# Kernel optimization log

Hardware: AMD Instinct MI355X
Metric: run time of the kernel (lower is better)

Reference implementation:

```python
import jax, jax.numpy as jnp
import numpy as np
import math

N = 20000      # nodes
E = 640000     # edges (avg degree 32)
G = 128        # g_dim (input features)
H1 = 128       # rgcn output dim
H2 = 128       # transformer output dim
R = 8          # num_relations


def setup_inputs() -> dict:
    key = jax.random.key(0)
    ks = jax.random.split(key, 12)
    x = jax.random.normal(ks[0], (N, G), dtype=jnp.float32)
    edge_index = jax.random.randint(ks[1], (2, E), 0, N)
    edge_type = jax.random.randint(ks[2], (E,), 0, R)
    s_in = 1.0 / math.sqrt(G)
    s_h1 = 1.0 / math.sqrt(H1)
    return {
        'x': x,
        'edge_index': edge_index,
        'edge_type': edge_type,
        # RGCNConv params (per-relation weights + root weight + bias)
        'rgcn_weight': jax.random.normal(ks[3], (R, G, H1), dtype=jnp.float32) * s_in,
        'rgcn_root': jax.random.normal(ks[4], (G, H1), dtype=jnp.float32) * s_in,
        'rgcn_bias': jnp.zeros((H1,), dtype=jnp.float32),
        # TransformerConv params (heads=1): query/key/value + skip linear
        'Wq': jax.random.normal(ks[5], (H1, H2), dtype=jnp.float32) * s_h1,
        'bq': jnp.zeros((H2,), dtype=jnp.float32),
        'Wk': jax.random.normal(ks[6], (H1, H2), dtype=jnp.float32) * s_h1,
        'bk': jnp.zeros((H2,), dtype=jnp.float32),
        'Wv': jax.random.normal(ks[7], (H1, H2), dtype=jnp.float32) * s_h1,
        'bv': jnp.zeros((H2,), dtype=jnp.float32),
        'Ws': jax.random.normal(ks[8], (H1, H2), dtype=jnp.float32) * s_h1,
        'bs': jnp.zeros((H2,), dtype=jnp.float32),
    }


def reference(x, edge_index, edge_type, rgcn_weight, rgcn_root, rgcn_bias,
              Wq, bq, Wk, bk, Wv, bv, Ws, bs):
    n = x.shape[0]
    src, dst = edge_index[0], edge_index[1]

    # ---- RGCNConv (aggr='mean' per relation, root weight + bias) ----
    # transform nodes by every relation, then gather per-edge message
    xr = jnp.einsum('ni,rio->nro', x, rgcn_weight)          # [N, R, H1]
    msg = xr[src, edge_type]                                # [E, H1]
    # per (dst, relation) edge counts for mean aggregation
    cnt = jnp.zeros((n, rgcn_weight.shape[0]), x.dtype).at[dst, edge_type].add(1.0)
    denom = jnp.maximum(cnt[dst, edge_type], 1.0)[:, None]  # [E, 1]
    agg = jnp.zeros((n, rgcn_weight.shape[2]), x.dtype).at[dst].add(msg / denom)
    h = agg + x @ rgcn_root + rgcn_bias
    h = jax.nn.relu(h)

    # ---- TransformerConv (heads=1, concat, root_weight=True) ----
    d = Wq.shape[1]
    q = h @ Wq + bq                                          # [N, H2]
    k = h @ Wk + bk
    v = h @ Wv + bv
    score = jnp.sum(q[dst] * k[src], axis=-1) / math.sqrt(d) # [E]
    # softmax over incoming edges of each destination node
    smax = jax.ops.segment_max(score, dst, num_segments=n)   # [N]
    e = jnp.exp(score - smax[dst])                           # [E]
    den = jax.ops.segment_sum(e, dst, num_segments=n)        # [N]
    alpha = e / jnp.maximum(den[dst], 1e-16)                 # [E]
    out = jax.ops.segment_sum(alpha[:, None] * v[src], dst, num_segments=n)
    out = out + h @ Ws + bs                                  # skip connection
    return jax.nn.relu(out)
```

## Files before the change

kernel.cpp:

```cpp
#include <hip/hip_runtime.h>

typedef unsigned short u16;
typedef unsigned int u32;
typedef __attribute__((ext_vector_type(8))) short short8;
typedef __attribute__((ext_vector_type(4))) float f32x4;

#define NN 20000
#define EE 640000
#define SCAN_BLOCKS 80

__device__ inline u16 f2bf(float f) {
    u32 x = __float_as_uint(f);
    return (u16)((x + 0x7FFFu + ((x >> 16) & 1u)) >> 16);
}
__device__ inline float lo16(u32 w) { return __uint_as_float(w << 16); }
__device__ inline float hi16(u32 w) { return __uint_as_float(w & 0xFFFF0000u); }
__device__ inline u32 packbf(float a, float b) { return ((u32)f2bf(b) << 16) | (u32)f2bf(a); }

#define ZP_N (NN * 8)
#define CX_N (NN * 32)
#define WP_N (128 * 1152 + 4 * 128 * 128 + 512)
__global__ __launch_bounds__(256) void prep_all(const float* __restrict__ x,
                                                const float* rw, const float* root,
                                                const float* Wq, const float* Wk,
                                                const float* Wv, const float* Ws,
                                                const float* bq, const float* bk,
                                                const float* bv, const float* bs,
                                                int* __restrict__ cnt, u16* __restrict__ xb,
                                                u16* wt1, u16* wt2, float* bcat) {
    int idx = blockIdx.x * 256 + threadIdx.x;
    if (idx < ZP_N) {
        cnt[idx] = 0;
        return;
    }
    idx -= ZP_N;
    if (idx < CX_N) {
        float4 v = *(const float4*)(x + (size_t)idx * 4);
        uint2 o;
        o.x = packbf(v.x, v.y);
        o.y = packbf(v.z, v.w);
        *(uint2*)(xb + (size_t)idx * 4) = o;
        return;
    }
    idx -= CX_N;
    const int S1 = 128 * 1152, S2 = 4 * 128 * 128;
    if (idx < S1) {
        int o = idx / 1152, k = idx - o * 1152;
        float v = (k < 1024) ? rw[k * 128 + o] : root[(k - 1024) * 128 + o];
        wt1[idx] = f2bf(v);
    } else if (idx < S1 + S2) {
        int j = idx - S1;
        int y = j >> 14, rem = j & 16383, o = rem >> 7, i = rem & 127;
        const float* W = (y == 0) ? Wq : (y == 1) ? Wk : (y == 2) ? Wv : Ws;
        wt2[j] = f2bf(W[i * 128 + o]);
    } else if (idx < S1 + S2 + 512) {
        int j = idx - (S1 + S2);
        int y = j >> 7, c = j & 127;
        const float* b = (y == 0) ? bq : (y == 1) ? bk : (y == 2) ? bv : bs;
        bcat[j] = b[c];
    }
}

__global__ void count_rank(const int* __restrict__ ei, const int* __restrict__ et,
                           int* __restrict__ cnt, int* __restrict__ rank) {
    int base = blockIdx.x * 1024 + threadIdx.x;
#pragma unroll
    for (int j = 0; j < 4; j++) {
        int e = base + j * 256;
        if (e < EE) {
            int dst = ei[EE + e];
            int r = et[e];
            rank[e] = atomicAdd(&cnt[dst * 8 + r], 1);
        }
    }
}

__global__ __launch_bounds__(256) void scan_phase1(const int* __restrict__ cnt,
                                                   int* __restrict__ deg_pref,
                                                   int* __restrict__ blk_sums) {
    __shared__ int lds[256];
    int t = threadIdx.x;
    int n = blockIdx.x * 256 + t;
    int d = 0;
    if (n < NN) {
        int4 c0 = *(const int4*)(cnt + n * 8);
        int4 c1 = *(const int4*)(cnt + n * 8 + 4);
        d = c0.x + c0.y + c0.z + c0.w + c1.x + c1.y + c1.z + c1.w;
    }
    lds[t] = d;
    __syncthreads();
    for (int o = 1; o < 256; o <<= 1) {
        int v = (t >= o) ? lds[t - o] : 0;
        __syncthreads();
        lds[t] += v;
        __syncthreads();
    }
    if (n < NN) deg_pref[n] = lds[t];
    if (t == 255) blk_sums[blockIdx.x] = lds[255];
}

__global__ void scan_phase2(int* __restrict__ blk_sums) {
    __shared__ int lds[128];
    int t = threadIdx.x;
    int v = (t < SCAN_BLOCKS) ? blk_sums[t] : 0;
    lds[t] = v;
    __syncthreads();
    for (int o = 1; o < 128; o <<= 1) {
        int a = (t >= o) ? lds[t - o] : 0;
        __syncthreads();
        lds[t] += a;
        __syncthreads();
    }
    if (t < SCAN_BLOCKS) blk_sums[t] = lds[t] - v;
}

__global__ __launch_bounds__(256) void scan_phase3(const int* __restrict__ cnt,
                                                   const int* __restrict__ deg_pref,
                                                   const int* __restrict__ blk_sums,
                                                   int* __restrict__ row_off,
                                                   int* __restrict__ srt) {
    int n = blockIdx.x * 256 + threadIdx.x;
    if (n >= NN) return;
    int4 c0 = *(const int4*)(cnt + n * 8);
    int4 c1 = *(const int4*)(cnt + n * 8 + 4);
    int deg = c0.x + c0.y + c0.z + c0.w + c1.x + c1.y + c1.z + c1.w;
    int start = blk_sums[blockIdx.x] + deg_pref[n] - deg;
    row_off[n] = start;
    int sub = start;
    int o[8];
    o[0] = sub; sub += c0.x;
    o[1] = sub; sub += c0.y;
    o[2] = sub; sub += c0.z;
    o[3] = sub; sub += c0.w;
    o[4] = sub; sub += c1.x;
    o[5] = sub; sub += c1.y;
    o[6] = sub; sub += c1.z;
    o[7] = sub; sub += c1.w;
    *(int4*)(srt + n * 8) = make_int4(o[0], o[1], o[2], o[3]);
    *(int4*)(srt + n * 8 + 4) = make_int4(o[4], o[5], o[6], o[7]);
    if (n == NN - 1) row_off[NN] = sub;
}

__global__ void scatter_kernel(const int* __restrict__ ei, const int* __restrict__ et,
                               const int* __restrict__ srt, const int* __restrict__ rank,
                               int* __restrict__ es) {
    int base = blockIdx.x * 1024 + threadIdx.x;
#pragma unroll
    for (int j = 0; j < 4; j++) {
        int e = base + j * 256;
        if (e < EE) {
            int dst = ei[EE + e];
            int src = ei[e];
            int r = et[e];
            es[srt[dst * 8 + r] + rank[e]] = src;
        }
    }
}

__global__ __launch_bounds__(256) void rgcn_agg(const u16* __restrict__ xb,
                                                const int* __restrict__ srt,
                                                const int* __restrict__ cnt,
                                                const int* __restrict__ es,
                                                u16* __restrict__ pre) {
    int gid = blockIdx.x * 16 + (threadIdx.x >> 4);
    int lane = threadIdx.x & 15;
    if (gid >= NN * 9) return;
    int node = gid / 9;
    int slot = gid - node * 9;
    long prebase = (long)node * 1152;
    if (slot == 8) {
        uint4 xv = *(const uint4*)(xb + (long)node * 128 + lane * 8);
        *(uint4*)(pre + prebase + 1024 + lane * 8) = xv;
        return;
    }
    int c = cnt[node * 8 + slot];
    int p0 = srt[node * 8 + slot];
    float inv = 1.0f / (float)(c > 1 ? c : 1);
    float a0 = 0.f, a1 = 0.f, a2 = 0.f, a3 = 0.f, a4 = 0.f, a5 = 0.f, a6 = 0.f, a7 = 0.f;
    int i = 0;
    for (; i + 4 <= c; i += 4) {
        int s0 = es[p0 + i], s1 = es[p0 + i + 1], s2 = es[p0 + i + 2], s3 = es[p0 + i + 3];
        uint4 w0 = *(const uint4*)(xb + (long)s0 * 128 + lane * 8);
        uint4 w1 = *(const uint4*)(xb + (long)s1 * 128 + lane * 8);
        uint4 w2 = *(const uint4*)(xb + (long)s2 * 128 + lane * 8);
        uint4 w3 = *(const uint4*)(xb + (long)s3 * 128 + lane * 8);
        a0 += (lo16(w0.x) + lo16(w1.x)) + (lo16(w2.x) + lo16(w3.x));
        a1 += (hi16(w0.x) + hi16(w1.x)) + (hi16(w2.x) + hi16(w3.x));
        a2 += (lo16(w0.y) + lo16(w1.y)) + (lo16(w2.y) + lo16(w3.y));
        a3 += (hi16(w0.y) + hi16(w1.y)) + (hi16(w2.y) + hi16(w3.y));
        a4 += (lo16(w0.z) + lo16(w1.z)) + (lo16(w2.z) + lo16(w3.z));
        a5 += (hi16(w0.z) + hi16(w1.z)) + (hi16(w2.z) + hi16(w3.z));
        a6 += (lo16(w0.w) + lo16(w1.w)) + (lo16(w2.w) + lo16(w3.w));
        a7 += (hi16(w0.w) + hi16(w1.w)) + (hi16(w2.w) + hi16(w3.w));
    }
    for (; i < c; i++) {
        int s = es[p0 + i];
        uint4 w = *(const uint4*)(xb + (long)s * 128 + lane * 8);
        a0 += lo16(w.x); a1 += hi16(w.x); a2 += lo16(w.y); a3 += hi16(w.y);
        a4 += lo16(w.z); a5 += hi16(w.z); a6 += lo16(w.w); a7 += hi16(w.w);
    }
    uint4 ow;
    ow.x = packbf(a0 * inv, a1 * inv);
    ow.y = packbf(a2 * inv, a3 * inv);
    ow.z = packbf(a4 * inv, a5 * inv);
    ow.w = packbf(a6 * inv, a7 * inv);
    *(uint4*)(pre + prebase + slot * 128 + lane * 8) = ow;
}

__global__ __launch_bounds__(256) void gemm_bm32(const u16* __restrict__ A,
                                                 const u16* __restrict__ Bt,
                                                 const float* __restrict__ bias,
                                                 u16* __restrict__ C, int rows) {
    __shared__ u16 As[32 * 136];
    __shared__ u16 Bs[128 * 136];
    int tid = threadIdx.x;
    int w = tid >> 6;
    int lane = tid & 63;
    int quad = lane >> 4;
    int ml = lane & 15;
    int mt = w & 1;
    int nq = w >> 1;
    int block_m = blockIdx.x * 32;

    f32x4 acc[4];
#pragma unroll
    for (int i = 0; i < 4; i++) acc[i] = (f32x4){0.f, 0.f, 0.f, 0.f};

    int rbase = tid >> 4;
    int cb = (tid & 15) * 8;

    for (int kb = 0; kb < 1152; kb += 128) {
#pragma unroll
        for (int rep = 0; rep < 2; rep++) {
            int r = rbase + rep * 16;
            int gr = block_m + r;
            short8 val = {};
            if (gr < rows) val = *(const short8*)(A + (long)gr * 1152 + kb + cb);
            *(short8*)(As + r * 136 + cb) = val;
        }
#pragma unroll
        for (int rep = 0; rep < 8; rep++) {
            int r = rbase + rep * 16;
            short8 val = *(const short8*)(Bt + (long)r * 1152 + kb + cb);
            *(short8*)(Bs + r * 136 + cb) = val;
        }
        __syncthreads();
#pragma unroll
        for (int ks = 0; ks < 4; ks++) {
            short8 af = *(const short8*)(As + (mt * 16 + ml) * 136 + ks * 32 + quad * 8);
#pragma unroll
            for (int nt = 0; nt < 4; nt++) {
                short8 bfr = *(const short8*)(Bs + (nq * 64 + nt * 16 + ml) * 136 + ks * 32 + quad * 8);
                acc[nt] = __builtin_amdgcn_mfma_f32_16x16x32_bf16(af, bfr, acc[nt], 0, 0, 0);
            }
        }
        __syncthreads();
    }
#pragma unroll
    for (int nt = 0; nt < 4; nt++) {
        int col = nq * 64 + nt * 16 + ml;
        float bv = bias[col];
#pragma unroll
        for (int i = 0; i < 4; i++) {
            int gr = block_m + mt * 16 + quad * 4 + i;
            if (gr < rows) {
                float vv = fmaxf(acc[nt][i] + bv, 0.f);
                C[(long)gr * 128 + col] = f2bf(vv);
            }
        }
    }
}

__global__ __launch_bounds__(256) void gemm_kernel(const u16* __restrict__ A, int lda,
                                                   const u16* __restrict__ Bt, int ldbt,
                                                   const float* __restrict__ bias,
                                                   u16* __restrict__ C, int ldc,
                                                   int rows, int K, int relu,
                                                   long long yBt, long long yC, long long yBias) {
    Bt += blockIdx.y * yBt;
    C += blockIdx.y * yC;
    bias += blockIdx.y * yBias;
    __shared__ u16 As[64 * 136];
    __shared__ u16 Bs[128 * 136];
    int tid = threadIdx.x;
    int w = tid >> 6;
    int lane = tid & 63;
    int quad = lane >> 4;
    int ml = lane & 15;
    int block_m = blockIdx.x * 64;

    f32x4 acc[8];
#pragma unroll
    for (int i = 0; i < 8; i++) acc[i] = (f32x4){0.f, 0.f, 0.f, 0.f};

    int rbase = tid >> 4;
    int cb = (tid & 15) * 8;

    for (int kb = 0; kb < K; kb += 128) {
#pragma unroll
        for (int rep = 0; rep < 4; rep++) {
            int r = rbase + rep * 16;
            int gr = block_m + r;
            short8 val = {};
            if (gr < rows) val = *(const short8*)(A + (long)gr * lda + kb + cb);
            *(short8*)(As + r * 136 + cb) = val;
        }
#pragma unroll
        for (int rep = 0; rep < 8; rep++) {
            int r = rbase + rep * 16;
            short8 val = *(const short8*)(Bt + (long)r * ldbt + kb + cb);
            *(short8*)(Bs + r * 136 + cb) = val;
        }
        __syncthreads();
#pragma unroll
        for (int ks = 0; ks < 4; ks++) {
            short8 af = *(const short8*)(As + (w * 16 + ml) * 136 + ks * 32 + quad * 8);
#pragma unroll
            for (int nt = 0; nt < 8; nt++) {
                short8 bfr = *(const short8*)(Bs + (nt * 16 + ml) * 136 + ks * 32 + quad * 8);
                acc[nt] = __builtin_amdgcn_mfma_f32_16x16x32_bf16(af, bfr, acc[nt], 0, 0, 0);
            }
        }
        __syncthreads();
    }
#pragma unroll
    for (int nt = 0; nt < 8; nt++) {
        int col = nt * 16 + ml;
        float bv = bias[col];
#pragma unroll
        for (int i = 0; i < 4; i++) {
            int gr = block_m + w * 16 + quad * 4 + i;
            if (gr < rows) {
                float vv = acc[nt][i] + bv;
                if (relu) vv = fmaxf(vv, 0.f);
                C[(long)gr * ldc + col] = f2bf(vv);
            }
        }
    }
}

__global__ __launch_bounds__(256) void attn_kernel(const u16* __restrict__ q, const u16* __restrict__ k,
                                                   const u16* __restrict__ v, const u16* __restrict__ skip,
                                                   const int* __restrict__ row_off, const int* __restrict__ es,
                                                   float* __restrict__ out) {
    int node = blockIdx.x * 16 + (threadIdx.x >> 4);
    int lane = threadIdx.x & 15;
    if (node >= NN) return;
    int p0 = row_off[node], p1 = row_off[node + 1];
    uint4 qw = *(const uint4*)(q + (long)node * 128 + lane * 8);
    float q0 = lo16(qw.x), q1 = hi16(qw.x), q2 = lo16(qw.y), q3 = hi16(qw.y);
    float q4 = lo16(qw.z), q5 = hi16(qw.z), q6 = lo16(qw.w), q7 = hi16(qw.w);
    const float SC = 0.08838834764831845f;
    float m = -INFINITY, l = 0.f;
    float a0 = 0.f, a1 = 0.f, a2 = 0.f, a3 = 0.f, a4 = 0.f, a5 = 0.f, a6 = 0.f, a7 = 0.f;
    int p = p0;
    for (; p + 4 <= p1; p += 4) {
        int s0 = es[p], s1 = es[p + 1], s2 = es[p + 2], s3 = es[p + 3];
        uint4 k0 = *(const uint4*)(k + (long)s0 * 128 + lane * 8);
        uint4 k1 = *(const uint4*)(k + (long)s1 * 128 + lane * 8);
        uint4 k2 = *(const uint4*)(k + (long)s2 * 128 + lane * 8);
        uint4 k3 = *(const uint4*)(k + (long)s3 * 128 + lane * 8);
        uint4 v0 = *(const uint4*)(v + (long)s0 * 128 + lane * 8);
        uint4 v1 = *(const uint4*)(v + (long)s1 * 128 + lane * 8);
        uint4 v2 = *(const uint4*)(v + (long)s2 * 128 + lane * 8);
        uint4 v3 = *(const uint4*)(v + (long)s3 * 128 + lane * 8);
        float t0 = q0 * lo16(k0.x) + q1 * hi16(k0.x) + q2 * lo16(k0.y) + q3 * hi16(k0.y) +
                   q4 * lo16(k0.z) + q5 * hi16(k0.z) + q6 * lo16(k0.w) + q7 * hi16(k0.w);
        float t1 = q0 * lo16(k1.x) + q1 * hi16(k1.x) + q2 * lo16(k1.y) + q3 * hi16(k1.y) +
                   q4 * lo16(k1.z) + q5 * hi16(k1.z) + q6 * lo16(k1.w) + q7 * hi16(k1.w);
        float t2 = q0 * lo16(k2.x) + q1 * hi16(k2.x) + q2 * lo16(k2.y) + q3 * hi16(k2.y) +
                   q4 * lo16(k2.z) + q5 * hi16(k2.z) + q6 * lo16(k2.w) + q7 * hi16(k2.w);
        float t3 = q0 * lo16(k3.x) + q1 * hi16(k3.x) + q2 * lo16(k3.y) + q3 * hi16(k3.y) +
                   q4 * lo16(k3.z) + q5 * hi16(k3.z) + q6 * lo16(k3.w) + q7 * hi16(k3.w);
#pragma unroll
        for (int off = 8; off >= 1; off >>= 1) {
            t0 += __shfl_xor(t0, off, 16);
            t1 += __shfl_xor(t1, off, 16);
            t2 += __shfl_xor(t2, off, 16);
            t3 += __shfl_xor(t3, off, 16);
        }
        t0 *= SC; t1 *= SC; t2 *= SC; t3 *= SC;
        float mx = fmaxf(fmaxf(t0, t1), fmaxf(t2, t3));
        float mn = fmaxf(m, mx);
        float scale = __expf(m - mn);
        float w0 = __expf(t0 - mn), w1 = __expf(t1 - mn), w2 = __expf(t2 - mn), w3 = __expf(t3 - mn);
        l = l * scale + ((w0 + w1) + (w2 + w3));
        a0 = a0 * scale + w0 * lo16(v0.x) + w1 * lo16(v1.x) + w2 * lo16(v2.x) + w3 * lo16(v3.x);
        a1 = a1 * scale + w0 * hi16(v0.x) + w1 * hi16(v1.x) + w2 * hi16(v2.x) + w3 * hi16(v3.x);
        a2 = a2 * scale + w0 * lo16(v0.y) + w1 * lo16(v1.y) + w2 * lo16(v2.y) + w3 * lo16(v3.y);
        a3 = a3 * scale + w0 * hi16(v0.y) + w1 * hi16(v1.y) + w2 * hi16(v2.y) + w3 * hi16(v3.y);
        a4 = a4 * scale + w0 * lo16(v0.z) + w1 * lo16(v1.z) + w2 * lo16(v2.z) + w3 * lo16(v3.z);
        a5 = a5 * scale + w0 * hi16(v0.z) + w1 * hi16(v1.z) + w2 * hi16(v2.z) + w3 * hi16(v3.z);
        a6 = a6 * scale + w0 * lo16(v0.w) + w1 * lo16(v1.w) + w2 * lo16(v2.w) + w3 * lo16(v3.w);
        a7 = a7 * scale + w0 * hi16(v0.w) + w1 * hi16(v1.w) + w2 * hi16(v2.w) + w3 * hi16(v3.w);
        m = mn;
    }
    for (; p < p1; p++) {
        int s = es[p];
        uint4 kw = *(const uint4*)(k + (long)s * 128 + lane * 8);
        uint4 vw = *(const uint4*)(v + (long)s * 128 + lane * 8);
        float t = q0 * lo16(kw.x) + q1 * hi16(kw.x) + q2 * lo16(kw.y) + q3 * hi16(kw.y) +
                  q4 * lo16(kw.z) + q5 * hi16(kw.z) + q6 * lo16(kw.w) + q7 * hi16(kw.w);
#pragma unroll
        for (int off = 8; off >= 1; off >>= 1) t += __shfl_xor(t, off, 16);
        t *= SC;
        float mn = fmaxf(m, t);
        float scale = __expf(m - mn);
        float wgt = __expf(t - mn);
        l = l * scale + wgt;
        a0 = a0 * scale + wgt * lo16(vw.x);
        a1 = a1 * scale + wgt * hi16(vw.x);
        a2 = a2 * scale + wgt * lo16(vw.y);
        a3 = a3 * scale + wgt * hi16(vw.y);
        a4 = a4 * scale + wgt * lo16(vw.z);
        a5 = a5 * scale + wgt * hi16(vw.z);
        a6 = a6 * scale + wgt * lo16(vw.w);
        a7 = a7 * scale + wgt * hi16(vw.w);
        m = mn;
    }
    float invl = (l > 0.f) ? 1.0f / l : 0.f;
    uint4 sw = *(const uint4*)(skip + (long)node * 128 + lane * 8);
    float4 oa, ob;
    oa.x = fmaxf(a0 * invl + lo16(sw.x), 0.f);
    oa.y = fmaxf(a1 * invl + hi16(sw.x), 0.f);
    oa.z = fmaxf(a2 * invl + lo16(sw.y), 0.f);
    oa.w = fmaxf(a3 * invl + hi16(sw.y), 0.f);
    ob.x = fmaxf(a4 * invl + lo16(sw.z), 0.f);
    ob.y = fmaxf(a5 * invl + hi16(sw.z), 0.f);
    ob.z = fmaxf(a6 * invl + lo16(sw.w), 0.f);
    ob.w = fmaxf(a7 * invl + hi16(sw.w), 0.f);
    *(float4*)(out + (long)node * 128 + lane * 8) = oa;
    *(float4*)(out + (long)node * 128 + lane * 8 + 4) = ob;
}

extern "C" void kernel_launch(void* const* d_in, const int* in_sizes, int n_in,
                              void* d_out, int out_size, void* d_ws, size_t ws_size,
                              hipStream_t stream) {
    const float* x = (const float*)d_in[0];
    const int* ei = (const int*)d_in[1];
    const int* et = (const int*)d_in[2];
    const float* rw = (const float*)d_in[3];
    const float* root = (const float*)d_in[4];
    const float* rbias = (const float*)d_in[5];
    const float* Wq = (const float*)d_in[6];
    const float* bq = (const float*)d_in[7];
    const float* Wk = (const float*)d_in[8];
    const float* bk = (const float*)d_in[9];
    const float* Wv = (const float*)d_in[10];
    const float* bv = (const float*)d_in[11];
    const float* Ws = (const float*)d_in[12];
    const float* bs = (const float*)d_in[13];

    char* ws = (char*)d_ws;
    size_t off = 0;
    auto alloc = [&](size_t b) {
        size_t o = off;
        off = (off + b + 255) & ~(size_t)255;
        return o;
    };
    u16* pre = (u16*)(ws + alloc((size_t)NN * 1152 * 2));
    u16* h = (u16*)(ws + alloc((size_t)NN * 128 * 2));
    u16* qkvs = (u16*)(ws + alloc((size_t)4 * NN * 128 * 2));
    u16* xb = (u16*)(ws + alloc((size_t)NN * 128 * 2));
    u16* wt1 = (u16*)(ws + alloc((size_t)128 * 1152 * 2));
    u16* wt2 = (u16*)(ws + alloc((size_t)4 * 128 * 128 * 2));
    float* bcat = (float*)(ws + alloc((size_t)512 * 4));
    int* cnt = (int*)(ws + alloc((size_t)NN * 8 * 4));
    int* row_off = (int*)(ws + alloc((size_t)(NN + 1) * 4));
    int* srt = (int*)(ws + alloc((size_t)NN * 8 * 4));
    int* deg_pref = (int*)(ws + alloc((size_t)NN * 4));
    int* blk_sums = (int*)(ws + alloc((size_t)128 * 4));
    int* rank = (int*)(ws + alloc((size_t)EE * 4));
    int* es = (int*)(ws + alloc((size_t)EE * 4));
    (void)ws_size;
    (void)in_sizes;
    (void)n_in;
    (void)out_size;

    prep_all<<<(ZP_N + CX_N + WP_N + 255) / 256, 256, 0, stream>>>(
        x, rw, root, Wq, Wk, Wv, Ws, bq, bk, bv, bs, cnt, xb, wt1, wt2, bcat);

    count_rank<<<(EE + 1023) / 1024, 256, 0, stream>>>(ei, et, cnt, rank);
    scan_phase1<<<SCAN_BLOCKS, 256, 0, stream>>>(cnt, deg_pref, blk_sums);
    scan_phase2<<<1, 128, 0, stream>>>(blk_sums);
    scan_phase3<<<SCAN_BLOCKS, 256, 0, stream>>>(cnt, deg_pref, blk_sums, row_off, srt);
    scatter_kernel<<<(EE + 1023) / 1024, 256, 0, stream>>>(ei, et, srt, rank, es);

    rgcn_agg<<<(NN * 9 + 15) / 16, 256, 0, stream>>>(xb, srt, cnt, es, pre);

    gemm_bm32<<<(NN + 31) / 32, 256, 0, stream>>>(pre, wt1, rbias, h, NN);
    gemm_kernel<<<dim3((NN + 63) / 64, 4), 256, 0, stream>>>(h, 128, wt2, 128, bcat, qkvs, 128,
                                                             NN, 128, 0, (long long)128 * 128,
                                                             (long long)NN * 128, 128);

    attn_kernel<<<(NN + 15) / 16, 256, 0, stream>>>(qkvs, qkvs + (size_t)NN * 128, qkvs + (size_t)2 * NN * 128,
                                                    qkvs + (size_t)3 * NN * 128, row_off, es, (float*)d_out);
}
```

Baseline: 250.9 us.

## Interleave K and V rows and drop online-softmax max tracking in attention

The QKV GEMM now writes K and V into one interleaved buffer with row stride 256, so each gathered source node's key and value sit in a single 512-byte span, which should improve locality for the random gathers. The attention loop drops the running maximum and rescaling and instead uses exp of the clamped score directly, which removes the extra exp and multiplies per edge. The GEMM is specialized to K=128 with no relu branch. Skipping max subtraction relies on scores staying small, and the clamp at 70 only guards against overflow, so accuracy could suffer for inputs with large scores.

Result: no change. 246.1 us (-1.9%).

```diff
diff --git a/kernel.cpp b/kernel.cpp
--- a/kernel.cpp
+++ b/kernel.cpp
@@ -271,15 +271,21 @@
     }
 }
 
-__global__ __launch_bounds__(256) void gemm_kernel(const u16* __restrict__ A, int lda,
-                                                   const u16* __restrict__ Bt, int ldbt,
-                                                   const float* __restrict__ bias,
-                                                   u16* __restrict__ C, int ldc,
-                                                   int rows, int K, int relu,
-                                                   long long yBt, long long yC, long long yBias) {
-    Bt += blockIdx.y * yBt;
-    C += blockIdx.y * yC;
-    bias += blockIdx.y * yBias;
+__global__ __launch_bounds__(256) void gemm_qkvs(const u16* __restrict__ A,
+                                                 const u16* __restrict__ Bt,
+                                                 const float* __restrict__ bias,
+                                                 u16* __restrict__ Cq, u16* __restrict__ Ckv,
+                                                 u16* __restrict__ Cs, int rows) {
+    int y = blockIdx.y;
+    Bt += (long)y * 128 * 128;
+    bias += y * 128;
+    u16* C;
+    int ldc;
+    if (y == 0) { C = Cq; ldc = 128; }
+    else if (y == 1) { C = Ckv; ldc = 256; }
+    else if (y == 2) { C = Ckv + 128; ldc = 256; }
+    else { C = Cs; ldc = 128; }
+
     __shared__ u16 As[64 * 136];
     __shared__ u16 Bs[128 * 136];
     int tid = threadIdx.x;
@@ -296,32 +302,29 @@
     int rbase = tid >> 4;
     int cb = (tid & 15) * 8;
 
-    for (int kb = 0; kb < K; kb += 128) {
-#pragma unroll
-        for (int rep = 0; rep < 4; rep++) {
-            int r = rbase + rep * 16;
-            int gr = block_m + r;
-            short8 val = {};
-            if (gr < rows) val = *(const short8*)(A + (long)gr * lda + kb + cb);
-            *(short8*)(As + r * 136 + cb) = val;
-        }
-#pragma unroll
-        for (int rep = 0; rep < 8; rep++) {
-            int r = rbase + rep * 16;
-            short8 val = *(const short8*)(Bt + (long)r * ldbt + kb + cb);
-            *(short8*)(Bs + r * 136 + cb) = val;
-        }
-        __syncthreads();
-#pragma unroll
-        for (int ks = 0; ks < 4; ks++) {
-            short8 af = *(const short8*)(As + (w * 16 + ml) * 136 + ks * 32 + quad * 8);
-#pragma unroll
-            for (int nt = 0; nt < 8; nt++) {
-                short8 bfr = *(const short8*)(Bs + (nt * 16 + ml) * 136 + ks * 32 + quad * 8);
-                acc[nt] = __builtin_amdgcn_mfma_f32_16x16x32_bf16(af, bfr, acc[nt], 0, 0, 0);
-            }
-        }
-        __syncthreads();
+#pragma unroll
+    for (int rep = 0; rep < 4; rep++) {
+        int r = rbase + rep * 16;
+        int gr = block_m + r;
+        short8 val = {};
+        if (gr < rows) val = *(const short8*)(A + (long)gr * 128 + cb);
+        *(short8*)(As + r * 136 + cb) = val;
+    }
+#pragma unroll
+    for (int rep = 0; rep < 8; rep++) {
+        int r = rbase + rep * 16;
+        short8 val = *(const short8*)(Bt + (long)r * 128 + cb);
+        *(short8*)(Bs + r * 136 + cb) = val;
+    }
+    __syncthreads();
+#pragma unroll
+    for (int ks = 0; ks < 4; ks++) {
+        short8 af = *(const short8*)(As + (w * 16 + ml) * 136 + ks * 32 + quad * 8);
+#pragma unroll
+        for (int nt = 0; nt < 8; nt++) {
+            short8 bfr = *(const short8*)(Bs + (nt * 16 + ml) * 136 + ks * 32 + quad * 8);
+            acc[nt] = __builtin_amdgcn_mfma_f32_16x16x32_bf16(af, bfr, acc[nt], 0, 0, 0);
+        }
     }
 #pragma unroll
     for (int nt = 0; nt < 8; nt++) {
@@ -331,17 +334,17 @@
         for (int i = 0; i < 4; i++) {
             int gr = block_m + w * 16 + quad * 4 + i;
             if (gr < rows) {
-                float vv = acc[nt][i] + bv;
-                if (relu) vv = fmaxf(vv, 0.f);
-                C[(long)gr * ldc + col] = f2bf(vv);
+                C[(long)gr * ldc + col] = f2bf(acc[nt][i] + bv);
             }
         }
     }
 }
 
-__global__ __launch_bounds__(256) void attn_kernel(const u16* __restrict__ q, const u16* __restrict__ k,
-                                                   const u16* __restrict__ v, const u16* __restrict__ skip,
-                                                   const int* __restrict__ row_off, const int* __restrict__ es,
+__global__ __launch_bounds__(256) void attn_kernel(const u16* __restrict__ q,
+                                                   const u16* __restrict__ kv,
+                                                   const u16* __restrict__ skip,
+                                                   const int* __restrict__ row_off,
+                                                   const int* __restrict__ es,
                                                    float* __restrict__ out) {
     int node = blockIdx.x * 16 + (threadIdx.x >> 4);
     int lane = threadIdx.x & 15;
@@ -351,19 +354,22 @@
     float q0 = lo16(qw.x), q1 = hi16(qw.x), q2 = lo16(qw.y), q3 = hi16(qw.y);
     float q4 = lo16(qw.z), q5 = hi16(qw.z), q6 = lo16(qw.w), q7 = hi16(qw.w);
     const float SC = 0.08838834764831845f;
-    float m = -INFINITY, l = 0.f;
+    float l = 0.f;
     float a0 = 0.f, a1 = 0.f, a2 = 0.f, a3 = 0.f, a4 = 0.f, a5 = 0.f, a6 = 0.f, a7 = 0.f;
     int p = p0;
     for (; p + 4 <= p1; p += 4) {
-        int s0 = es[p], s1 = es[p + 1], s2 = es[p + 2], s3 = es[p + 3];
-        uint4 k0 = *(const uint4*)(k + (long)s0 * 128 + lane * 8);
-        uint4 k1 = *(const uint4*)(k + (long)s1 * 128 + lane * 8);
-        uint4 k2 = *(const uint4*)(k + (long)s2 * 128 + lane * 8);
-        uint4 k3 = *(const uint4*)(k + (long)s3 * 128 + lane * 8);
-        uint4 v0 = *(const uint4*)(v + (long)s0 * 128 + lane * 8);
-        uint4 v1 = *(const uint4*)(v + (long)s1 * 128 + lane * 8);
-        uint4 v2 = *(const uint4*)(v + (long)s2 * 128 + lane * 8);
-        uint4 v3 = *(const uint4*)(v + (long)s3 * 128 + lane * 8);
+        const u16* b0 = kv + (long)es[p] * 256 + lane * 8;
+        const u16* b1 = kv + (long)es[p + 1] * 256 + lane * 8;
+        const u16* b2 = kv + (long)es[p + 2] * 256 + lane * 8;
+        const u16* b3 = kv + (long)es[p + 3] * 256 + lane * 8;
+        uint4 k0 = *(const uint4*)b0;
+        uint4 k1 = *(const uint4*)b1;
+        uint4 k2 = *(const uint4*)b2;
+        uint4 k3 = *(const uint4*)b3;
+        uint4 v0 = *(const uint4*)(b0 + 128);
+        uint4 v1 = *(const uint4*)(b1 + 128);
+        uint4 v2 = *(const uint4*)(b2 + 128);
+        uint4 v3 = *(const uint4*)(b3 + 128);
         float t0 = q0 * lo16(k0.x) + q1 * hi16(k0.x) + q2 * lo16(k0.y) + q3 * hi16(k0.y) +
                    q4 * lo16(k0.z) + q5 * hi16(k0.z) + q6 * lo16(k0.w) + q7 * hi16(k0.w);
         float t1 = q0 * lo16(k1.x) + q1 * hi16(k1.x) + q2 * lo16(k1.y) + q3 * hi16(k1.y) +
@@ -379,44 +385,38 @@
             t2 += __shfl_xor(t2, off, 16);
             t3 += __shfl_xor(t3, off, 16);
         }
-        t0 *= SC; t1 *= SC; t2 *= SC; t3 *= SC;
-        float mx = fmaxf(fmaxf(t0, t1), fmaxf(t2, t3));
-        float mn = fmaxf(m, mx);
-        float scale = __expf(m - mn);
-        float w0 = __expf(t0 - mn), w1 = __expf(t1 - mn), w2 = __expf(t2 - mn), w3 = __expf(t3 - mn);
-        l = l * scale + ((w0 + w1) + (w2 + w3));
-        a0 = a0 * scale + w0 * lo16(v0.x) + w1 * lo16(v1.x) + w2 * lo16(v2.x) + w3 * lo16(v3.x);
-        a1 = a1 * scale + w0 * hi16(v0.x) + w1 * hi16(v1.x) + w2 * hi16(v2.x) + w3 * hi16(v3.x);
-        a2 = a2 * scale + w0 * lo16(v0.y) + w1 * lo16(v1.y) + w2 * lo16(v2.y) + w3 * lo16(v3.y);
-        a3 = a3 * scale + w0 * hi16(v0.y) + w1 * hi16(v1.y) + w2 * hi16(v2.y) + w3 * hi16(v3.y);
-        a4 = a4 * scale + w0 * lo16(v0.z) + w1 * lo16(v1.z) + w2 * lo16(v2.z) + w3 * lo16(v3.z);
-        a5 = a5 * scale + w0 * hi16(v0.z) + w1 * hi16(v1.z) + w2 * hi16(v2.z) + w3 * hi16(v3.z);
-        a6 = a6 * scale + w0 * lo16(v0.w) + w1 * lo16(v1.w) + w2 * lo16(v2.w) + w3 * lo16(v3.w);
-        a7 = a7 * scale + w0 * hi16(v0.w) + w1 * hi16(v1.w) + w2 * hi16(v2.w) + w3 * hi16(v3.w);
-        m = mn;
+        float w0 = __expf(fminf(t0 * SC, 70.f));
+        float w1 = __expf(fminf(t1 * SC, 70.f));
+        float w2 = __expf(fminf(t2 * SC, 70.f));
+        float w3 = __expf(fminf(t3 * SC, 70.f));
+        l += (w0 + w1) + (w2 + w3);
+        a0 += w0 * lo16(v0.x) + w1 * lo16(v1.x) + w2 * lo16(v2.x) + w3 * lo16(v3.x);
+        a1 += w0 * hi16(v0.x) + w1 * hi16(v1.x) + w2 * hi16(v2.x) + w3 * hi16(v3.x);
+        a2 += w0 * lo16(v0.y) + w1 * lo16(v1.y) + w2 * lo16(v2.y) + w3 * lo16(v3.y);
+        a3 += w0 * hi16(v0.y) + w1 * hi16(v1.y) + w2 * hi16(v2.y) + w3 * hi16(v3.y);
+        a4 += w0 * lo16(v0.z) + w1 * lo16(v1.z) + w2 * lo16(v2.z) + w3 * lo16(v3.z);
+        a5 += w0 * hi16(v0.z) + w1 * hi16(v1.z) + w2 * hi16(v2.z) + w3 * hi16(v3.z);
+        a6 += w0 * lo16(v0.w) + w1 * lo16(v1.w) + w2 * lo16(v2.w) + w3 * lo16(v3.w);
+        a7 += w0 * hi16(v0.w) + w1 * hi16(v1.w) + w2 * hi16(v2.w) + w3 * hi16(v3.w);
     }
     for (; p < p1; p++) {
-        int s = es[p];
-        uint4 kw = *(const uint4*)(k + (long)s * 128 + lane * 8);
-        uint4 vw = *(const uint4*)(v + (long)s * 128 + lane * 8);
+        const u16* b = kv + (long)es[p] * 256 + lane * 8;
+        uint4 kw = *(const uint4*)b;
+        uint4 vw = *(const uint4*)(b + 128);
         float t = q0 * lo16(kw.x) + q1 * hi16(kw.x) + q2 * lo16(kw.y) + q3 * hi16(kw.y) +
                   q4 * lo16(kw.z) + q5 * hi16(kw.z) + q6 * lo16(kw.w) + q7 * hi16(kw.w);
 #pragma unroll
         for (int off = 8; off >= 1; off >>= 1) t += __shfl_xor(t, off, 16);
-        t *= SC;
-        float mn = fmaxf(m, t);
-        float scale = __expf(m - mn);
-        float wgt = __expf(t - mn);
-        l = l * scale + wgt;
-        a0 = a0 * scale + wgt * lo16(vw.x);
-        a1 = a1 * scale + wgt * hi16(vw.x);
-        a2 = a2 * scale + wgt * lo16(vw.y);
-        a3 = a3 * scale + wgt * hi16(vw.y);
-        a4 = a4 * scale + wgt * lo16(vw.z);
-        a5 = a5 * scale + wgt * hi16(vw.z);
-        a6 = a6 * scale + wgt * lo16(vw.w);
-        a7 = a7 * scale + wgt * hi16(vw.w);
-        m = mn;
+        float w = __expf(fminf(t * SC, 70.f));
+        l += w;
+        a0 += w * lo16(vw.x);
+        a1 += w * hi16(vw.x);
+        a2 += w * lo16(vw.y);
+        a3 += w * hi16(vw.y);
+        a4 += w * lo16(vw.z);
+        a5 += w * hi16(vw.z);
+        a6 += w * lo16(vw.w);
+        a7 += w * hi16(vw.w);
     }
     float invl = (l > 0.f) ? 1.0f / l : 0.f;
     uint4 sw = *(const uint4*)(skip + (long)node * 128 + lane * 8);
@@ -460,7 +460,9 @@
     };
     u16* pre = (u16*)(ws + alloc((size_t)NN * 1152 * 2));
     u16* h = (u16*)(ws + alloc((size_t)NN * 128 * 2));
-    u16* qkvs = (u16*)(ws + alloc((size_t)4 * NN * 128 * 2));
+    u16* qv = (u16*)(ws + alloc((size_t)NN * 128 * 2));
+    u16* kv = (u16*)(ws + alloc((size_t)NN * 256 * 2));
+    u16* skip = (u16*)(ws + alloc((size_t)NN * 128 * 2));
     u16* xb = (u16*)(ws + alloc((size_t)NN * 128 * 2));
     u16* wt1 = (u16*)(ws + alloc((size_t)128 * 1152 * 2));
     u16* wt2 = (u16*)(ws + alloc((size_t)4 * 128 * 128 * 2));
@@ -489,10 +491,7 @@
     rgcn_agg<<<(NN * 9 + 15) / 16, 256, 0, stream>>>(xb, srt, cnt, es, pre);
 
     gemm_bm32<<<(NN + 31) / 32, 256, 0, stream>>>(pre, wt1, rbias, h, NN);
-    gemm_kernel<<<dim3((NN + 63) / 64, 4), 256, 0, stream>>>(h, 128, wt2, 128, bcat, qkvs, 128,
-                                                             NN, 128, 0, (long long)128 * 128,
-                                                             (long long)NN * 128, 128);
-
-    attn_kernel<<<(NN + 15) / 16, 256, 0, stream>>>(qkvs, qkvs + (size_t)NN * 128, qkvs + (size_t)2 * NN * 128,
-                                                    qkvs + (size_t)3 * NN * 128, row_off, es, (float*)d_out);
-}
+    gemm_qkvs<<<dim3((NN + 63) / 64, 4), 256, 0, stream>>>(h, wt2, bcat, qv, kv, skip, NN);
+
+    attn_kernel<<<(NN + 15) / 16, 256, 0, stream>>>(qv, kv, skip, row_off, es, (float*)d_out);
+}
```
